# Performance work log

Hardware: AMD Instinct MI355X
Metric: run time of the kernel (lower is better)

## Reference

```python
import jax, jax.numpy as jnp
import numpy as np

NUM_HEADS = 16
NUM_KV_HEADS = 4
HEAD_DIM = 128
HALF_DIM = HEAD_DIM // 2
LAMBDA_INIT = 0.8
LAMBDA_MIN = 0.0
LAMBDA_MAX = 1.0
CAUSAL = True
NORMALIZE_DIFF = True
NEG = -1.0e9


def setup_inputs() -> dict:
    key = jax.random.key(0)
    k1, k2, k3 = jax.random.split(key, 3)
    B, Sq, Sk = 1, 2048, 2048
    query = jax.random.normal(k1, (B, NUM_HEADS, Sq, HEAD_DIM), dtype=jnp.float32)
    key_t = jax.random.normal(k2, (B, NUM_KV_HEADS, Sk, HEAD_DIM), dtype=jnp.float32)
    value = jax.random.normal(k3, (B, NUM_KV_HEADS, Sk, HEAD_DIM), dtype=jnp.float32)
    return {"query": query, "key": key_t, "value": value}


def reference(query, key, value):
    scale = 1.0 / (HALF_DIM ** 0.5)
    lam = jnp.clip(jnp.float32(LAMBDA_INIT), LAMBDA_MIN, LAMBDA_MAX)
    # GQA: repeat KV heads to match query heads
    rep = NUM_HEADS // NUM_KV_HEADS
    k = jnp.repeat(key, rep, axis=1)    # [b,h,k,d]
    v = jnp.repeat(value, rep, axis=1)  # [b,h,k,d]
    q1, q2 = query[..., :HALF_DIM], query[..., HALF_DIM:]
    k1, k2 = k[..., :HALF_DIM], k[..., HALF_DIM:]
    scores1 = jnp.einsum('bhqd,bhkd->bhqk', q1, k1) * scale
    scores2 = jnp.einsum('bhqd,bhkd->bhqk', q2, k2) * scale
    if CAUSAL:
        Sq, Sk = query.shape[2], k.shape[2]
        mask = jnp.tril(jnp.ones((Sq, Sk), dtype=jnp.float32))  # lower-triangular causal
        scores1 = scores1 * mask + (1.0 - mask) * NEG
        scores2 = scores2 * mask + (1.0 - mask) * NEG
    attn1 = jax.nn.softmax(scores1, axis=-1)
    attn2 = jax.nn.softmax(scores2, axis=-1)
    diff_attn = attn1 - lam * attn2
    out = jnp.einsum('bhqk,bhkd->bhqd', diff_attn, v)
    if NORMALIZE_DIFF:
        out = out * (1.0 - LAMBDA_INIT)
    return out
```

## Files before the change

kernel.cpp:

```cpp
#include <hip/hip_runtime.h>

#define NUM_HEADS 16
#define HEAD_DIM  128
#define SEQ       2048
#define KT_STRIDE 8192

typedef __attribute__((ext_vector_type(8))) unsigned short us8;
typedef __attribute__((ext_vector_type(8))) __bf16 bf16x8;
typedef __attribute__((ext_vector_type(4))) float f32x4;
typedef __attribute__((ext_vector_type(16))) float f32x16;
typedef __attribute__((ext_vector_type(4))) unsigned u32x4;

static __device__ inline unsigned short f2bf(float x) {
    union { float f; unsigned u; } v; v.f = x;
    unsigned r = v.u + 0x7FFFu + ((v.u >> 16) & 1u);
    return (unsigned short)(r >> 16);
}
static __device__ inline unsigned pk2bf(float a, float b) {
    return (unsigned)f2bf(a) | ((unsigned)f2bf(b) << 16);
}
static __device__ inline float fast_exp2(float x) {
#if __has_builtin(__builtin_amdgcn_exp2f)
    return __builtin_amdgcn_exp2f(x);
#else
    return exp2f(x);
#endif
}
static __device__ inline unsigned pack_hi(unsigned clo, unsigned chi) {
#if __has_builtin(__builtin_amdgcn_perm)
    return __builtin_amdgcn_perm(chi, clo, 0x07060302u);
#else
    return (clo >> 16) | (chi & 0xffff0000u);
#endif
}
static __device__ inline f32x16 mfma32(us8 a, us8 b, f32x16 c) {
    return __builtin_amdgcn_mfma_f32_32x32x16_bf16(
        __builtin_bit_cast(bf16x8, a), __builtin_bit_cast(bf16x8, b), c, 0, 0, 0);
}

__global__ __launch_bounds__(256)
void prep_frag(const float* __restrict__ K, const float* __restrict__ V,
               unsigned short* __restrict__ KF, unsigned short* __restrict__ VF)
{
    const int bx  = (int)blockIdx.x, t = (int)threadIdx.x;
    const int which = bx & 1, kt = (bx >> 1) & 31, kvh = bx >> 6;
    __shared__ __align__(16) float Ls[64][132];

    const float* src = (which ? V : K) + ((size_t)kvh * SEQ + kt * 64) * HEAD_DIM;
    #pragma unroll
    for (int i = 0; i < 8; ++i) {
        const int idx = t + i * 256;
        const int r = idx >> 5, c4 = idx & 31;
        *(float4*)&Ls[r][c4 * 4] = *(const float4*)(src + (size_t)r * HEAD_DIM + c4 * 4);
    }
    __syncthreads();

    if (!which) {
        #pragma unroll
        for (int i = 0; i < 4; ++i) {
            const int c = t + i * 256;
            const int lane = c & 63, ds = (c >> 6) & 3, mat = (c >> 8) & 1, kh = c >> 9;
            const int H = lane >> 5;
            const int row = kh * 32 + (lane & 31);
            const int dim = mat * 64 + ds * 16 + H * 8;
            u32x4 pk;
            #pragma unroll
            for (int jj = 0; jj < 4; ++jj)
                pk[jj] = pk2bf(Ls[row][dim + 2*jj], Ls[row][dim + 2*jj + 1]);
            *(us8*)(KF + ((size_t)(kvh * 32 + kt) * 16 + kh * 8 + mat * 4 + ds) * 512 + lane * 8)
                = __builtin_bit_cast(us8, pk);
        }
    } else {
        #pragma unroll
        for (int i = 0; i < 4; ++i) {
            const int c = t + i * 256;
            const int lane = c & 63, db = (c >> 6) & 3, ks = (c >> 8) & 1, kh = c >> 9;
            const int H = lane >> 5;
            const int s0 = kh * 32 + ks * 16 + H * 8;
            const int d  = db * 32 + (lane & 31);
            u32x4 pk;
            #pragma unroll
            for (int jj = 0; jj < 4; ++jj)
                pk[jj] = pk2bf(Ls[s0 + 2*jj][d], Ls[s0 + 2*jj + 1][d]);
            *(us8*)(VF + ((size_t)(kvh * 32 + kt) * 16 + kh * 8 + ks * 4 + db) * 512 + lane * 8)
                = __builtin_bit_cast(us8, pk);
        }
    }
}

__global__ __launch_bounds__(256, 2)
void diff_attn_mfma10(const float* __restrict__ Q,
                      const unsigned short* __restrict__ KF,
                      const unsigned short* __restrict__ VF,
                      float* __restrict__ Out)
{
    __shared__ float cb[2][32][136];
    __shared__ float rsb[2][2][32];

    const int t   = (int)threadIdx.x;
    const int wv  = t >> 6;
    const int ln  = t & 63;
    const int mat = wv >> 1;
    const int kh  = wv & 1;
    const int q   = ln & 31;
    const int H   = ln >> 5;

    const int bx   = (int)blockIdx.x;
    const int h    = bx & 15;
    const int idx  = bx >> 4;
    const int qtA  = idx, qtB = 63 - idx;
    const int nktA = (qtA >> 1) + 1;
    const int kvh  = h >> 2;

    const unsigned short* kfb = KF + ((size_t)kvh * 32 * 16 + kh * 8 + mat * 4) * 512 + ln * 8;
    const unsigned short* vfb = VF + ((size_t)kvh * 32 * 16 + kh * 8) * 512 + ln * 8;

    const float qscale = 0.125f * 1.44269504088896340736f;

    us8 qhi[4];
    auto loadQ = [&](int q0c) {
        const float* qr = Q + ((size_t)h * SEQ + q0c + q) * HEAD_DIM + mat * 64;
        #pragma unroll
        for (int ds = 0; ds < 4; ++ds) {
            const int d0 = ds * 16 + H * 8;
            float x[8];
            *(float4*)&x[0] = *(const float4*)(qr + d0);
            *(float4*)&x[4] = *(const float4*)(qr + d0 + 4);
            us8 hi8;
            #pragma unroll
            for (int j = 0; j < 8; ++j) hi8[j] = f2bf(x[j] * qscale);
            qhi[ds] = hi8;
        }
    };

    f32x16 o[4];
    f32x4  rsv;

    auto epilogue = [&](int q0c) {
        __syncthreads();
        float rsc = (rsv[0] + rsv[1]) + (rsv[2] + rsv[3]);
        rsc += __shfl_xor(rsc, 32, 64);
        if (ln < 32) rsb[mat][kh][ln] = rsc;
        if (kh == 1) {
            #pragma unroll
            for (int db = 0; db < 4; ++db)
                #pragma unroll
                for (int i = 0; i < 4; ++i) {
                    float4 v = { o[db][i*4+0], o[db][i*4+1], o[db][i*4+2], o[db][i*4+3] };
                    *(float4*)&cb[mat][q][db * 32 + 8 * i + 4 * H] = v;
                }
        }
        __syncthreads();
        if (kh == 0) {
            const float l = rsb[mat][0][q] + rsb[mat][1][q];
            const float a = mat ? (0.16f / l) : (0.2f / l);
            #pragma unroll
            for (int db = 0; db < 4; ++db)
                #pragma unroll
                for (int i = 0; i < 4; ++i) {
                    float4 v = *(float4*)&cb[mat][q][db * 32 + 8 * i + 4 * H];
                    o[db][i*4+0] = (o[db][i*4+0] + v.x) * a;
                    o[db][i*4+1] = (o[db][i*4+1] + v.y) * a;
                    o[db][i*4+2] = (o[db][i*4+2] + v.z) * a;
                    o[db][i*4+3] = (o[db][i*4+3] + v.w) * a;
                }
            if (mat == 1) {
                #pragma unroll
                for (int db = 0; db < 4; ++db)
                    #pragma unroll
                    for (int i = 0; i < 4; ++i) {
                        float4 v = { o[db][i*4+0], o[db][i*4+1], o[db][i*4+2], o[db][i*4+3] };
                        *(float4*)&cb[1][q][db * 32 + 8 * i + 4 * H] = v;
                    }
            }
        }
        __syncthreads();
        if (wv == 0) {
            float* ob = Out + ((size_t)h * SEQ + q0c + q) * HEAD_DIM;
            #pragma unroll
            for (int db = 0; db < 4; ++db)
                #pragma unroll
                for (int i = 0; i < 4; ++i) {
                    float4 v = *(float4*)&cb[1][q][db * 32 + 8 * i + 4 * H];
                    float4 r;
                    r.x = o[db][i*4+0] - v.x;
                    r.y = o[db][i*4+1] - v.y;
                    r.z = o[db][i*4+2] - v.z;
                    r.w = o[db][i*4+3] - v.w;
                    *(float4*)(ob + db * 32 + 8 * i + 4 * H) = r;
                }
        }
    };

    auto run_seg = [&](int q0c, int nseg) {
        us8 kaA[4], kaB[4];

        auto body = [&](int j, us8 (&kaIn)[4], us8 (&kaOut)[4], f32x16& sIn, f32x16& sOut) {
            us8 va[8];
            {
                const unsigned short* vb = vfb + (size_t)j * KT_STRIDE;
                #pragma unroll
                for (int c = 0; c < 8; ++c) va[c] = *(const us8*)(vb + c * 512);
            }
            if (j + 2 < nseg) {
                const unsigned short* kb = kfb + (size_t)(j + 2) * KT_STRIDE;
                #pragma unroll
                for (int ds = 0; ds < 4; ++ds) kaOut[ds] = *(const us8*)(kb + ds * 512);
            }
            sOut = (f32x16)0.f;
            if (j + 1 < nseg) {
                #pragma unroll
                for (int ds = 0; ds < 4; ++ds) sOut = mfma32(kaIn[ds], qhi[ds], sOut);
            }
            unsigned c[16];
            if (j == nseg - 1) {
                const int kg0 = j * 64 + kh * 32 + 4 * H;
                const int qg  = q0c + q;
                #pragma unroll
                for (int r = 0; r < 16; ++r) {
                    const int kg = kg0 + (r & 3) + ((r >> 2) << 3);
                    float e = (kg <= qg) ? fast_exp2(sIn[r]) : 0.f;
                    c[r] = __builtin_bit_cast(unsigned, e);
                }
            } else {
                #pragma unroll
                for (int r = 0; r < 16; ++r)
                    c[r] = __builtin_bit_cast(unsigned, fast_exp2(sIn[r]));
            }
            #pragma unroll
            for (int ks = 0; ks < 2; ++ks) {
                const unsigned pA = pack_hi(c[8*ks+0], c[8*ks+1]);
                const unsigned pB = pack_hi(c[8*ks+2], c[8*ks+3]);
                const unsigned pC = pack_hi(c[8*ks+4], c[8*ks+5]);
                const unsigned pD = pack_hi(c[8*ks+6], c[8*ks+7]);
                rsv[0] += __builtin_bit_cast(float, pA << 16);
                rsv[1] += __builtin_bit_cast(float, pA & 0xffff0000u);
                rsv[2] += __builtin_bit_cast(float, pB << 16);
                rsv[3] += __builtin_bit_cast(float, pB & 0xffff0000u);
                rsv[0] += __builtin_bit_cast(float, pC << 16);
                rsv[1] += __builtin_bit_cast(float, pC & 0xffff0000u);
                rsv[2] += __builtin_bit_cast(float, pD << 16);
                rsv[3] += __builtin_bit_cast(float, pD & 0xffff0000u);
                const unsigned x1 = H ? pA : pC;
                const unsigned x2 = H ? pB : pD;
                const unsigned t1 = (unsigned)__shfl_xor((int)x1, 32, 64);
                const unsigned t2 = (unsigned)__shfl_xor((int)x2, 32, 64);
                u32x4 bw;
                bw[0] = H ? t1 : pA;
                bw[1] = H ? t2 : pB;
                bw[2] = H ? pC : t1;
                bw[3] = H ? pD : t2;
                const us8 bp = __builtin_bit_cast(us8, bw);
                #pragma unroll
                for (int db = 0; db < 4; ++db)
                    o[db] = mfma32(va[ks * 4 + db], bp, o[db]);
            }
        };

        f32x16 s0, s1;
        #pragma unroll
        for (int ds = 0; ds < 4; ++ds) kaA[ds] = *(const us8*)(kfb + ds * 512);
        s0 = (f32x16)0.f;
        #pragma unroll
        for (int ds = 0; ds < 4; ++ds) s0 = mfma32(kaA[ds], qhi[ds], s0);
        if (nseg > 1) {
            #pragma unroll
            for (int ds = 0; ds < 4; ++ds) kaA[ds] = *(const us8*)(kfb + KT_STRIDE + ds * 512);
        }

        int j = 0;
        for (; j + 2 <= nseg; j += 2) {
            body(j,     kaA, kaB, s0, s1);
            body(j + 1, kaB, kaA, s1, s0);
        }
        if (j < nseg) body(j, kaA, kaB, s0, s1);
    };

    loadQ(qtA * 32);
    #pragma unroll
    for (int i = 0; i < 4; ++i) o[i] = (f32x16)0.f;
    rsv = (f32x4)0.f;
    run_seg(qtA * 32, nktA);
    epilogue(qtA * 32);

    loadQ(qtB * 32);
    #pragma unroll
    for (int i = 0; i < 4; ++i) o[i] = (f32x16)0.f;
    rsv = (f32x4)0.f;
    run_seg(qtB * 32, 33 - nktA);
    epilogue(qtB * 32);
}

extern "C" void kernel_launch(void* const* d_in, const int* in_sizes, int n_in,
                              void* d_out, int out_size, void* d_ws, size_t ws_size,
                              hipStream_t stream) {
    const float* Q = (const float*)d_in[0];
    const float* K = (const float*)d_in[1];
    const float* V = (const float*)d_in[2];
    float* Out = (float*)d_out;

    unsigned short* KF = (unsigned short*)d_ws;
    unsigned short* VF = KF + (size_t)4 * SEQ * HEAD_DIM;

    prep_frag<<<256, 256, 0, stream>>>(K, V, KF, VF);
    diff_attn_mfma10<<<512, 256, 0, stream>>>(Q, KF, VF, Out);
}
```

Before: 111.8 us.

## Split paired query tiles into separate blocks, drop score software pipelining, use permlane32_swap

The attention kernel now gives each block a single query tile, longest first, instead of pairing tile A with tile 63-A. This doubles the grid to 1024 blocks and raises the launch-bounds occupancy target to 3. The one-step-ahead QK score pipelining is removed, which cuts register pressure at the cost of less MFMA/exp overlap. The half-wave exchange uses the permlane32_swap builtin when it is available, and the prep kernel is split over twice as many blocks with half-size tiles. The risk is load imbalance across causal tiles and exposed latency from the shallower pipeline.

```diff
diff --git a/kernel.cpp b/kernel.cpp
--- a/kernel.cpp
+++ b/kernel.cpp
@@ -10,6 +10,7 @@
 typedef __attribute__((ext_vector_type(4))) float f32x4;
 typedef __attribute__((ext_vector_type(16))) float f32x16;
 typedef __attribute__((ext_vector_type(4))) unsigned u32x4;
+typedef __attribute__((ext_vector_type(2))) unsigned u32x2;
 
 static __device__ inline unsigned short f2bf(float x) {
     union { float f; unsigned u; } v; v.f = x;
@@ -43,12 +44,12 @@
                unsigned short* __restrict__ KF, unsigned short* __restrict__ VF)
 {
     const int bx  = (int)blockIdx.x, t = (int)threadIdx.x;
-    const int which = bx & 1, kt = (bx >> 1) & 31, kvh = bx >> 6;
-    __shared__ __align__(16) float Ls[64][132];
-
-    const float* src = (which ? V : K) + ((size_t)kvh * SEQ + kt * 64) * HEAD_DIM;
+    const int which = bx & 1, khb = (bx >> 1) & 1, kt = (bx >> 2) & 31, kvh = bx >> 7;
+    __shared__ __align__(16) float Ls[32][132];
+
+    const float* src = (which ? V : K) + ((size_t)kvh * SEQ + kt * 64 + khb * 32) * HEAD_DIM;
     #pragma unroll
-    for (int i = 0; i < 8; ++i) {
+    for (int i = 0; i < 4; ++i) {
         const int idx = t + i * 256;
         const int r = idx >> 5, c4 = idx & 31;
         *(float4*)&Ls[r][c4 * 4] = *(const float4*)(src + (size_t)r * HEAD_DIM + c4 * 4);
@@ -57,39 +58,39 @@
 
     if (!which) {
         #pragma unroll
-        for (int i = 0; i < 4; ++i) {
+        for (int i = 0; i < 2; ++i) {
             const int c = t + i * 256;
-            const int lane = c & 63, ds = (c >> 6) & 3, mat = (c >> 8) & 1, kh = c >> 9;
+            const int lane = c & 63, ds = (c >> 6) & 3, mat = (c >> 8) & 1;
             const int H = lane >> 5;
-            const int row = kh * 32 + (lane & 31);
+            const int row = lane & 31;
             const int dim = mat * 64 + ds * 16 + H * 8;
             u32x4 pk;
             #pragma unroll
             for (int jj = 0; jj < 4; ++jj)
                 pk[jj] = pk2bf(Ls[row][dim + 2*jj], Ls[row][dim + 2*jj + 1]);
-            *(us8*)(KF + ((size_t)(kvh * 32 + kt) * 16 + kh * 8 + mat * 4 + ds) * 512 + lane * 8)
+            *(us8*)(KF + ((size_t)(kvh * 32 + kt) * 16 + khb * 8 + mat * 4 + ds) * 512 + lane * 8)
                 = __builtin_bit_cast(us8, pk);
         }
     } else {
         #pragma unroll
-        for (int i = 0; i < 4; ++i) {
+        for (int i = 0; i < 2; ++i) {
             const int c = t + i * 256;
-            const int lane = c & 63, db = (c >> 6) & 3, ks = (c >> 8) & 1, kh = c >> 9;
+            const int lane = c & 63, db = (c >> 6) & 3, ks = (c >> 8) & 1;
             const int H = lane >> 5;
-            const int s0 = kh * 32 + ks * 16 + H * 8;
+            const int s0 = ks * 16 + H * 8;
             const int d  = db * 32 + (lane & 31);
             u32x4 pk;
             #pragma unroll
             for (int jj = 0; jj < 4; ++jj)
                 pk[jj] = pk2bf(Ls[s0 + 2*jj][d], Ls[s0 + 2*jj + 1][d]);
-            *(us8*)(VF + ((size_t)(kvh * 32 + kt) * 16 + kh * 8 + ks * 4 + db) * 512 + lane * 8)
+            *(us8*)(VF + ((size_t)(kvh * 32 + kt) * 16 + khb * 8 + ks * 4 + db) * 512 + lane * 8)
                 = __builtin_bit_cast(us8, pk);
         }
     }
 }
 
-__global__ __launch_bounds__(256, 2)
-void diff_attn_mfma10(const float* __restrict__ Q,
+__global__ __launch_bounds__(256, 3)
+void diff_attn_mfma11(const float* __restrict__ Q,
                       const unsigned short* __restrict__ KF,
                       const unsigned short* __restrict__ VF,
                       float* __restrict__ Out)
@@ -105,12 +106,11 @@
     const int q   = ln & 31;
     const int H   = ln >> 5;
 
-    const int bx   = (int)blockIdx.x;
-    const int h    = bx & 15;
-    const int idx  = bx >> 4;
-    const int qtA  = idx, qtB = 63 - idx;
-    const int nktA = (qtA >> 1) + 1;
-    const int kvh  = h >> 2;
+    const int bx  = (int)blockIdx.x;
+    const int h   = bx & 15;
+    const int qt  = 63 - (bx >> 4);
+    const int nkt = (qt >> 1) + 1;
+    const int kvh = h >> 2;
 
     const unsigned short* kfb = KF + ((size_t)kvh * 32 * 16 + kh * 8 + mat * 4) * 512 + ln * 8;
     const unsigned short* vfb = VF + ((size_t)kvh * 32 * 16 + kh * 8) * 512 + ln * 8;
@@ -195,23 +195,22 @@
     auto run_seg = [&](int q0c, int nseg) {
         us8 kaA[4], kaB[4];
 
-        auto body = [&](int j, us8 (&kaIn)[4], us8 (&kaOut)[4], f32x16& sIn, f32x16& sOut) {
+        auto body = [&](int j, us8 (&kaIn)[4], us8 (&kaOut)[4]) {
             us8 va[8];
             {
                 const unsigned short* vb = vfb + (size_t)j * KT_STRIDE;
                 #pragma unroll
                 for (int c = 0; c < 8; ++c) va[c] = *(const us8*)(vb + c * 512);
             }
-            if (j + 2 < nseg) {
-                const unsigned short* kb = kfb + (size_t)(j + 2) * KT_STRIDE;
+            if (j + 1 < nseg) {
+                const unsigned short* kb = kfb + (size_t)(j + 1) * KT_STRIDE;
                 #pragma unroll
                 for (int ds = 0; ds < 4; ++ds) kaOut[ds] = *(const us8*)(kb + ds * 512);
             }
-            sOut = (f32x16)0.f;
-            if (j + 1 < nseg) {
-                #pragma unroll
-                for (int ds = 0; ds < 4; ++ds) sOut = mfma32(kaIn[ds], qhi[ds], sOut);
-            }
+            f32x16 s = (f32x16)0.f;
+            #pragma unroll
+            for (int ds = 0; ds < 4; ++ds) s = mfma32(kaIn[ds], qhi[ds], s);
+
             unsigned c[16];
             if (j == nseg - 1) {
                 const int kg0 = j * 64 + kh * 32 + 4 * H;
@@ -219,13 +218,13 @@
                 #pragma unroll
                 for (int r = 0; r < 16; ++r) {
                     const int kg = kg0 + (r & 3) + ((r >> 2) << 3);
-                    float e = (kg <= qg) ? fast_exp2(sIn[r]) : 0.f;
+                    float e = (kg <= qg) ? fast_exp2(s[r]) : 0.f;
                     c[r] = __builtin_bit_cast(unsigned, e);
                 }
             } else {
                 #pragma unroll
                 for (int r = 0; r < 16; ++r)
-                    c[r] = __builtin_bit_cast(unsigned, fast_exp2(sIn[r]));
+                    c[r] = __builtin_bit_cast(unsigned, fast_exp2(s[r]));
             }
             #pragma unroll
             for (int ks = 0; ks < 2; ++ks) {
@@ -241,15 +240,21 @@
                 rsv[1] += __builtin_bit_cast(float, pC & 0xffff0000u);
                 rsv[2] += __builtin_bit_cast(float, pD << 16);
                 rsv[3] += __builtin_bit_cast(float, pD & 0xffff0000u);
+                u32x4 bw;
+#if __has_builtin(__builtin_amdgcn_permlane32_swap)
+                u32x2 r02 = __builtin_amdgcn_permlane32_swap(pA, pC, false, false);
+                u32x2 r13 = __builtin_amdgcn_permlane32_swap(pB, pD, false, false);
+                bw[0] = r02[0]; bw[1] = r13[0]; bw[2] = r02[1]; bw[3] = r13[1];
+#else
                 const unsigned x1 = H ? pA : pC;
                 const unsigned x2 = H ? pB : pD;
                 const unsigned t1 = (unsigned)__shfl_xor((int)x1, 32, 64);
                 const unsigned t2 = (unsigned)__shfl_xor((int)x2, 32, 64);
-                u32x4 bw;
                 bw[0] = H ? t1 : pA;
                 bw[1] = H ? t2 : pB;
                 bw[2] = H ? pC : t1;
                 bw[3] = H ? pD : t2;
+#endif
                 const us8 bp = __builtin_bit_cast(us8, bw);
                 #pragma unroll
                 for (int db = 0; db < 4; ++db)
@@ -257,38 +262,23 @@
             }
         };
 
-        f32x16 s0, s1;
         #pragma unroll
         for (int ds = 0; ds < 4; ++ds) kaA[ds] = *(const us8*)(kfb + ds * 512);
-        s0 = (f32x16)0.f;
-        #pragma unroll
-        for (int ds = 0; ds < 4; ++ds) s0 = mfma32(kaA[ds], qhi[ds], s0);
-        if (nseg > 1) {
-            #pragma unroll
-            for (int ds = 0; ds < 4; ++ds) kaA[ds] = *(const us8*)(kfb + KT_STRIDE + ds * 512);
-        }
 
         int j = 0;
         for (; j + 2 <= nseg; j += 2) {
-            body(j,     kaA, kaB, s0, s1);
-            body(j + 1, kaB, kaA, s1, s0);
-        }
-        if (j < nseg) body(j, kaA, kaB, s0, s1);
+            body(j,     kaA, kaB);
+            body(j + 1, kaB, kaA);
+        }
+        if (j < nseg) body(j, kaA, kaB);
     };
 
-    loadQ(qtA * 32);
+    loadQ(qt * 32);
     #pragma unroll
     for (int i = 0; i < 4; ++i) o[i] = (f32x16)0.f;
     rsv = (f32x4)0.f;
-    run_seg(qtA * 32, nktA);
-    epilogue(qtA * 32);
-
-    loadQ(qtB * 32);
-    #pragma unroll
-    for (int i = 0; i < 4; ++i) o[i] = (f32x16)0.f;
-    rsv = (f32x4)0.f;
-    run_seg(qtB * 32, 33 - nktA);
-    epilogue(qtB * 32);
+    run_seg(qt * 32, nkt);
+    epilogue(qt * 32);
 }
 
 extern "C" void kernel_launch(void* const* d_in, const int* in_sizes, int n_in,
@@ -302,6 +292,6 @@
     unsigned short* KF = (unsigned short*)d_ws;
     unsigned short* VF = KF + (size_t)4 * SEQ * HEAD_DIM;
 
-    prep_frag<<<256, 256, 0, stream>>>(K, V, KF, VF);
-    diff_attn_mfma10<<<512, 256, 0, stream>>>(Q, KF, VF, Out);
-}
+    prep_frag<<<512, 256, 0, stream>>>(K, V, KF, VF);
+    diff_attn_mfma11<<<1024, 256, 0, stream>>>(Q, KF, VF, Out);
+}
```

Result: slower. 135.2 us (+20.9%).
